# Optimization experiments

Hardware: AMD Instinct MI355X
Metric: run time of the kernel (lower is better)

## Reference

```python
import jax, jax.numpy as jnp
import numpy as np

N, C, H, W, D = 2, 64, 256, 256, 2   # batch, dim, height, width, depth
NW, HEADS, TOPK, KVW = 8, 8, 4, 4    # n_win, num_heads, topk, kv_per_win


def _conv(x, w, b, pad, groups=1):
    # x: NCHW, w: OIHW
    y = jax.lax.conv_general_dilated(
        x, w, (1, 1), [(pad, pad), (pad, pad)],
        dimension_numbers=('NCHW', 'OIHW', 'NCHW'), feature_group_count=groups)
    return y if b is None else y + b[None, :, None, None]


def _ln(x, g, b):
    m = x.mean(-1, keepdims=True)
    v = ((x - m) ** 2).mean(-1, keepdims=True)
    return (x - m) * jax.lax.rsqrt(v + 1e-6) * g + b


def setup_inputs() -> dict:
    key = jax.random.key(0)
    ks = iter(jax.random.split(key, 32))
    def rn(shape, s=0.05):
        return jax.random.normal(next(ks), shape, jnp.float32) * s
    inp = {'x': jax.random.normal(next(ks), (N, C, H, W), jnp.float32)}
    inp.update(
        pos_w=rn((D, C, 1, 3, 3)), pos_b=jnp.zeros((D, C), jnp.float32),
        ln1_g=jnp.ones((D, C), jnp.float32), ln1_b=jnp.zeros((D, C), jnp.float32),
        qkv_w=rn((D, C, 3 * C)), qkv_b=jnp.zeros((D, 3 * C), jnp.float32),
        lepe_w=rn((D, C, 1, 5, 5)), lepe_b=jnp.zeros((D, C), jnp.float32),
        wo_w=rn((D, C, C)), wo_b=jnp.zeros((D, C), jnp.float32),
        ln2_g=jnp.ones((D, C), jnp.float32), ln2_b=jnp.zeros((D, C), jnp.float32),
        fc1_w=rn((D, C, 4 * C)), fc1_b=jnp.zeros((D, 4 * C), jnp.float32),
        pw_w=rn((D, 2 * C, 2 * C, 1, 1)),
        dw_w=rn((D, 2 * C, 1, 3, 3)), dw_b=jnp.zeros((D, 2 * C), jnp.float32),
        fc2_w=rn((D, 2 * C, C)), fc2_b=jnp.zeros((D, C), jnp.float32))
    return inp


def _attn(y, qkv_w, qkv_b, lepe_w, lepe_b, wo_w, wo_b):
    # Bi-level routing attention. y: NHWC
    n, h, w, c = y.shape
    hw, ww = h // NW, w // NW          # window size (32x32)
    p2 = NW * NW                        # number of windows (64)
    hd = c // HEADS
    scale = c ** -0.5                   # qk_dim ** -0.5
    qkv = y @ qkv_w + qkv_b             # (n,h,w,3c)
    q, kimg, vimg = jnp.split(qkv, 3, -1)

    def win(t):  # (n,h,w,c) -> (n,p2,hw,ww,c)
        return t.reshape(n, NW, hw, NW, ww, c).transpose(0, 1, 3, 2, 4, 5).reshape(n, p2, hw, ww, c)

    qw, kw, vw = win(q), win(kimg), win(vimg)
    # region-level routing: window-mean q/k, top-k windows per query window
    q_win = qw.mean((2, 3))
    k_win = kw.mean((2, 3))
    logits = jnp.einsum('npc,nqc->npq', q_win * scale, k_win)
    _, r_idx = jax.lax.top_k(logits, TOPK)           # (n,p2,topk) hard routing (mul_weight='none')
    # kv downsample: adaptive avg pool each 32x32 window to 4x4
    kv = jnp.concatenate([kw, vw], -1)               # (n,p2,hw,ww,2c)
    kvp = kv.reshape(n, p2, KVW, hw // KVW, KVW, ww // KVW, 2 * c).mean((3, 5))
    kvp = kvp.reshape(n, p2, KVW * KVW, 2 * c)       # (n,p2,16,2c)
    # gather top-k windows' kv tokens
    kv_sel = jax.vmap(lambda t, i: t[i])(kvp, r_idx)  # (n,p2,topk,16,2c)
    k_sel, v_sel = jnp.split(kv_sel, 2, -1)
    kt = TOPK * KVW * KVW                             # 64 kv tokens per window
    k_sel = k_sel.reshape(n, p2, kt, HEADS, hd)
    v_sel = v_sel.reshape(n, p2, kt, HEADS, hd)
    qp = qw.reshape(n, p2, hw * ww, HEADS, hd)
    att = jax.nn.softmax(jnp.einsum('npqhc,npkhc->nphqk', qp * scale, k_sel), -1)
    out = jnp.einsum('nphqk,npkhc->npqhc', att, v_sel).reshape(n, p2, hw, ww, c)
    out = out.reshape(n, NW, NW, hw, ww, c).transpose(0, 1, 3, 2, 4, 5).reshape(n, h, w, c)
    # LePE: depthwise 5x5 conv on v over the full image
    lepe = _conv(vimg.transpose(0, 3, 1, 2), lepe_w, lepe_b, 2, groups=c).transpose(0, 2, 3, 1)
    return (out + lepe) @ wo_w + wo_b


def _glu(y, fc1_w, fc1_b, pw_w, dw_w, dw_b, fc2_w, fc2_b):
    # BConvolutionalGLU. y: NHWC
    t = y @ fc1_w + fc1_b                 # (n,h,w,4c)
    xh, vh = jnp.split(t, 2, -1)          # each 2c
    xh = xh.transpose(0, 3, 1, 2)         # NCHW
    xh = _conv(xh, pw_w, None, 0)                           # BSConvU pointwise (no bias)
    xh = _conv(xh, dw_w, dw_b, 1, groups=dw_w.shape[0])     # BSConvU depthwise 3x3
    xh = jax.nn.gelu(xh, approximate=False) * vh.transpose(0, 3, 1, 2)
    return xh.transpose(0, 2, 3, 1) @ fc2_w + fc2_b


def reference(x, pos_w, pos_b, ln1_g, ln1_b, qkv_w, qkv_b, lepe_w, lepe_b,
              wo_w, wo_b, ln2_g, ln2_b, fc1_w, fc1_b, pw_w, dw_w, dw_b,
              fc2_w, fc2_b):
    for i in range(D):
        x = x + _conv(x, pos_w[i], pos_b[i], 1, groups=x.shape[1])
        y = x.transpose(0, 2, 3, 1)  # NHWC
        y = y + _attn(_ln(y, ln1_g[i], ln1_b[i]), qkv_w[i], qkv_b[i],
                      lepe_w[i], lepe_b[i], wo_w[i], wo_b[i])
        y = y + _glu(_ln(y, ln2_g[i], ln2_b[i]), fc1_w[i], fc1_b[i],
                     pw_w[i], dw_w[i], dw_b[i], fc2_w[i], fc2_b[i])
        x = y.transpose(0, 3, 1, 2)  # NCHW
    return x
```

## Files before the change

kernel.cpp:

```cpp
#include <hip/hip_runtime.h>
#include <hip/hip_bf16.h>

typedef __hip_bfloat16 bf16;
typedef __attribute__((ext_vector_type(8))) short short8v;
typedef __attribute__((ext_vector_type(4))) float f32x4;

static constexpr int Nn = 2, Hh = 256, Wd = 256;
static constexpr int Pp = Nn * Hh * Wd;

__device__ inline void sto(float* p, size_t i, float v) { p[i] = v; }
__device__ inline void sto(bf16* p, size_t i, float v) { p[i] = __float2bfloat16(v); }
__device__ inline void ld4(const float* p, float f[4]) {
  const float4 v = *(const float4*)p;
  f[0] = v.x; f[1] = v.y; f[2] = v.z; f[3] = v.w;
}
__device__ inline void ld4(const bf16* p, float f[4]) {
  uint2 u = *(const uint2*)p;
  f[0] = __uint_as_float(u.x << 16); f[1] = __uint_as_float(u.x & 0xffff0000u);
  f[2] = __uint_as_float(u.y << 16); f[3] = __uint_as_float(u.y & 0xffff0000u);
}
__device__ inline void st4(float* p, const float f[4]) {
  *(float4*)p = make_float4(f[0], f[1], f[2], f[3]);
}
__device__ inline void st4(bf16* p, const float f[4]) {
  union { bf16 h[4]; uint2 u; } x;
  x.h[0] = __float2bfloat16(f[0]); x.h[1] = __float2bfloat16(f[1]);
  x.h[2] = __float2bfloat16(f[2]); x.h[3] = __float2bfloat16(f[3]);
  *(uint2*)p = x.u;
}
__device__ inline uint2 pk4(float a, float b, float c, float d) {
  union { bf16 h[4]; uint2 u; } x;
  x.h[0] = __float2bfloat16(a); x.h[1] = __float2bfloat16(b);
  x.h[2] = __float2bfloat16(c); x.h[3] = __float2bfloat16(d);
  return x.u;
}

__global__ void __launch_bounds__(256) k_in_tr(const float* __restrict__ xin,
                                               float* __restrict__ X) {
  __shared__ float t[64][65];
  int blk = blockIdx.x;
  int wt = blk & 3, h = (blk >> 2) & 255, n = blk >> 10;
  int w0 = wt * 64;
  int tx = threadIdx.x & 63, ty = threadIdx.x >> 6;
  const float* src = xin + ((size_t)n * 64 * 256 + h) * 256 + w0;
#pragma unroll
  for (int cc = 0; cc < 16; cc++) {
    int c = cc * 4 + ty;
    t[c][tx] = src[(size_t)c * 65536 + tx];
  }
  __syncthreads();
  float* dst = X + (size_t)(n * 65536 + h * 256 + w0) * 64;
#pragma unroll
  for (int jj = 0; jj < 16; jj++) {
    int j = jj * 4 + ty;
    dst[(size_t)j * 64 + tx] = t[tx][j];
  }
}

__global__ void __launch_bounds__(256) k_out(const float* __restrict__ X,
                                             float* __restrict__ out) {
  __shared__ float t[64][65];
  int blk = blockIdx.x;
  int wt = blk & 3, h = (blk >> 2) & 255, n = blk >> 10;
  int w0 = wt * 64;
  int tx = threadIdx.x & 63, ty = threadIdx.x >> 6;
  const float* src = X + (size_t)(n * 65536 + h * 256 + w0) * 64;
#pragma unroll
  for (int jj = 0; jj < 16; jj++) {
    int j = jj * 4 + ty;
    t[tx][j] = src[(size_t)j * 64 + tx];
  }
  __syncthreads();
  float* dst = out + ((size_t)n * 64 * 256 + h) * 256 + w0;
#pragma unroll
  for (int cc = 0; cc < 16; cc++) {
    int c = cc * 4 + ty;
    dst[(size_t)c * 65536 + tx] = t[c][tx];
  }
}

__global__ void __launch_bounds__(256) k_pcln4(const float* __restrict__ X,
                                               float* __restrict__ A, float* __restrict__ T,
                                               bf16* __restrict__ Tb,
                                               const float* __restrict__ pw,
                                               const float* __restrict__ pb,
                                               const float* __restrict__ g,
                                               const float* __restrict__ b) {
  __shared__ float w9[9][68];
  __shared__ float bb[64];
  int tid = threadIdx.x;
  for (int j = tid; j < 576; j += 256) {
    int tap = j >> 6, c = j & 63;
    w9[tap][c] = pw[c * 9 + tap];
  }
  if (tid < 64) bb[tid] = pb[tid];
  __syncthreads();
  int gid = blockIdx.x * 256 + tid;
  int cg = gid & 15, pg = gid >> 4;
  int c0 = cg << 2;
  int w0 = (pg & 63) << 2, h = (pg >> 6) & 255, n = pg >> 14;
  int pbase = (n << 16) | (h << 8) | w0;
  float acc[4][4];
  {
    const float4 b4 = *(const float4*)&bb[c0];
#pragma unroll
    for (int px = 0; px < 4; px++) {
      acc[px][0] = b4.x; acc[px][1] = b4.y; acc[px][2] = b4.z; acc[px][3] = b4.w;
    }
  }
  float xc[4][4];
#pragma unroll
  for (int ky = 0; ky < 3; ky++) {
    int hh = h + ky - 1;
    if ((unsigned)hh >= 256u) continue;
    const float* xrow = X + (size_t)((n << 16) | (hh << 8)) * 64 + c0;
    float v[6][4];
#pragma unroll
    for (int dx = 0; dx < 6; dx++) {
      int ww = w0 + dx - 1;
      if ((unsigned)ww < 256u) ld4(xrow + (size_t)ww * 64, v[dx]);
      else { v[dx][0] = 0.f; v[dx][1] = 0.f; v[dx][2] = 0.f; v[dx][3] = 0.f; }
    }
    if (ky == 1) {
#pragma unroll
      for (int px = 0; px < 4; px++)
#pragma unroll
        for (int j = 0; j < 4; j++) xc[px][j] = v[px + 1][j];
    }
#pragma unroll
    for (int kx = 0; kx < 3; kx++) {
      const float4 wv = *(const float4*)&w9[ky * 3 + kx][c0];
#pragma unroll
      for (int px = 0; px < 4; px++) {
        acc[px][0] += wv.x * v[px + kx][0]; acc[px][1] += wv.y * v[px + kx][1];
        acc[px][2] += wv.z * v[px + kx][2]; acc[px][3] += wv.w * v[px + kx][3];
      }
    }
  }
  const float4 g4 = *(const float4*)&g[c0];
  const float4 b4 = *(const float4*)&b[c0];
#pragma unroll
  for (int px = 0; px < 4; px++) {
    float a[4];
#pragma unroll
    for (int j = 0; j < 4; j++) a[j] = xc[px][j] + acc[px][j];
    st4(A + (size_t)(pbase + px) * 64 + c0, a);
    float s = a[0] + a[1] + a[2] + a[3];
#pragma unroll
    for (int off = 8; off; off >>= 1) s += __shfl_xor(s, off);
    float mean = s * (1.f / 64.f);
    float d[4], q = 0.f;
#pragma unroll
    for (int j = 0; j < 4; j++) { d[j] = a[j] - mean; q += d[j] * d[j]; }
#pragma unroll
    for (int off = 8; off; off >>= 1) q += __shfl_xor(q, off);
    float inv = rsqrtf(q * (1.f / 64.f) + 1e-6f);
    float y[4] = {d[0] * inv * g4.x + b4.x, d[1] * inv * g4.y + b4.y,
                  d[2] * inv * g4.z + b4.z, d[3] * inv * g4.w + b4.w};
    st4(T + (size_t)(pbase + px) * 64 + c0, y);
    st4(Tb + (size_t)(pbase + px) * 64 + c0, y);
  }
}

__global__ void k_prep(const float* __restrict__ qkvw, const float* __restrict__ qkvb,
                       const float* __restrict__ wow, const float* __restrict__ f2w,
                       const float* __restrict__ f1w, const float* __restrict__ f1b,
                       const float* __restrict__ pww,
                       bf16* __restrict__ WTq, bf16* __restrict__ WTo,
                       bf16* __restrict__ WT2, bf16* __restrict__ WTf1,
                       float* __restrict__ qbs, float* __restrict__ bc) {
  int t = blockIdx.x * 256 + threadIdx.x;
  if (t < 8192) {
    int r = t >> 6, k = t & 63;
    int src = r < 64 ? r : r + 64;
    float v = qkvw[k * 192 + src];
    if (r < 64) v *= 0.125f;
    WTq[t] = __float2bfloat16(v);
  } else if (t < 12288) {
    int t2 = t - 8192;
    int r = t2 >> 6, k = t2 & 63;
    WTo[t2] = __float2bfloat16(wow[k * 64 + r]);
  } else if (t < 20480) {
    int t2 = t - 12288;
    int r = t2 >> 7, k = t2 & 127;
    WT2[t2] = __float2bfloat16(f2w[k * 64 + r]);
  } else if (t < 28672) {
    int t2 = t - 20480;
    int r = t2 >> 6, k = t2 & 63;
    WTf1[t2] = __float2bfloat16(f1w[k * 256 + 128 + r]);
  } else if (t < 36864) {
    int t2 = t - 28672;
    int o = t2 & 127, k = t2 >> 7;
    float acc = 0.f;
    for (int j = 0; j < 128; j++) acc += f1w[k * 256 + j] * pww[o * 128 + j];
    WTf1[(128 + o) * 64 + k] = __float2bfloat16(acc);
  } else if (t < 36992) {
    int o = t - 36864;
    float bv = 0.f;
    for (int j = 0; j < 128; j++) bv += f1b[j] * pww[o * 128 + j];
    bc[o] = bv;
  }
  if (t < 64) qbs[t] = qkvb[t] * 0.125f;
}

template <int K, int N1, int N2, typename TO1, typename TO2, bool RES>
__global__ void __launch_bounds__(256) k_mf(const bf16* __restrict__ In,
                                            const bf16* __restrict__ WT,
                                            const float* __restrict__ b1,
                                            const float* __restrict__ b2,
                                            const float* __restrict__ Res,
                                            TO1* __restrict__ O1, TO2* __restrict__ O2) {
  constexpr int NC = N1 + N2;
  constexpr int KS = K / 32;
  constexpr int NTW = NC / 64;
  constexpr int KB = K * 2;
  constexpr int CH = NC * K / 8;
  __shared__ char lw[NC * K * 2];
  int tid = threadIdx.x;
  for (int ch = tid; ch < CH; ch += 256) {
    int r = ch / (K / 8), cg = ch % (K / 8);
    int byte = (r * KB + cg * 16) ^ ((r & 7) << 4);
    *(uint4*)(lw + byte) = *(const uint4*)((const short*)WT + ch * 8);
  }
  __syncthreads();
  int wid = tid >> 6, lane = tid & 63;
  int lr = lane & 15, lg = lane >> 4;
  int mb = blockIdx.x * 128;
#pragma unroll 2
  for (int ms = 0; ms < 8; ms++) {
    int m0 = mb + ms * 16;
    short8v a[KS];
#pragma unroll
    for (int ks = 0; ks < KS; ks++)
      a[ks] = *(const short8v*)((const short*)In + (size_t)(m0 + lr) * K + ks * 32 + lg * 8);
#pragma unroll
    for (int t = 0; t < NTW; t++) {
      int nt = wid * NTW + t;
      int col = nt * 16 + lr;
      float bv = (N2 == 0 || col < N1) ? b1[col] : b2[col - N1];
      f32x4 acc = {bv, bv, bv, bv};
#pragma unroll
      for (int ks = 0; ks < KS; ks++) {
        int byte = (col * KB + ks * 64 + lg * 16) ^ ((col & 7) << 4);
        short8v bfrag = *(const short8v*)(lw + byte);
        acc = __builtin_amdgcn_mfma_f32_16x16x32_bf16(a[ks], bfrag, acc, 0, 0, 0);
      }
      int r0 = m0 + lg * 4;
#pragma unroll
      for (int j = 0; j < 4; j++) {
        float v = acc[j];
        size_t row = r0 + j;
        if (RES) v += Res[row * N1 + col];
        if (N2 == 0 || col < N1) sto(O1, row * N1 + col, v);
        else sto(O2, row * N2 + (col - N1), v);
      }
    }
  }
}

__global__ void __launch_bounds__(256) k_mf_wo_ln(const bf16* __restrict__ In,
                                                  const bf16* __restrict__ WT,
                                                  const float* __restrict__ bias,
                                                  const float* __restrict__ Res,
                                                  float* __restrict__ Xo,
                                                  bf16* __restrict__ A2b,
                                                  const float* __restrict__ g,
                                                  const float* __restrict__ b) {
  __shared__ char lw[64 * 64 * 2];
  __shared__ float xs[16][68];
  int tid = threadIdx.x;
  for (int ch = tid; ch < 512; ch += 256) {
    int r = ch >> 3, cg = ch & 7;
    int byte = (r * 128 + cg * 16) ^ ((r & 7) << 4);
    *(uint4*)(lw + byte) = *(const uint4*)((const short*)WT + ch * 8);
  }
  __syncthreads();
  int wid = tid >> 6, lane = tid & 63;
  int lr = lane & 15, lg = lane >> 4;
  int col = wid * 16 + lr;
  int mb = blockIdx.x * 128;
  int row2 = tid >> 4, cq = (tid & 15) << 2;
  const float4 g4 = *(const float4*)&g[cq];
  const float4 b4 = *(const float4*)&b[cq];
  float bv = bias[col];
  for (int ms = 0; ms < 8; ms++) {
    int m0 = mb + ms * 16;
    short8v a0 = *(const short8v*)((const short*)In + (size_t)(m0 + lr) * 64 + lg * 8);
    short8v a1 = *(const short8v*)((const short*)In + (size_t)(m0 + lr) * 64 + 32 + lg * 8);
    f32x4 acc = {bv, bv, bv, bv};
    {
      int byte = (col * 128 + lg * 16) ^ ((col & 7) << 4);
      acc = __builtin_amdgcn_mfma_f32_16x16x32_bf16(a0, *(const short8v*)(lw + byte), acc, 0, 0, 0);
      byte = (col * 128 + 64 + lg * 16) ^ ((col & 7) << 4);
      acc = __builtin_amdgcn_mfma_f32_16x16x32_bf16(a1, *(const short8v*)(lw + byte), acc, 0, 0, 0);
    }
    int r0 = m0 + lg * 4;
#pragma unroll
    for (int j = 0; j < 4; j++) {
      float v = acc[j] + Res[(size_t)(r0 + j) * 64 + col];
      Xo[(size_t)(r0 + j) * 64 + col] = v;
      xs[lg * 4 + j][col] = v;
    }
    __syncthreads();
    {
      float a4[4] = {xs[row2][cq], xs[row2][cq + 1], xs[row2][cq + 2], xs[row2][cq + 3]};
      float s = a4[0] + a4[1] + a4[2] + a4[3];
#pragma unroll
      for (int off = 8; off; off >>= 1) s += __shfl_xor(s, off);
      float mean = s * (1.f / 64.f);
      float d[4], q = 0.f;
#pragma unroll
      for (int j = 0; j < 4; j++) { d[j] = a4[j] - mean; q += d[j] * d[j]; }
#pragma unroll
      for (int off = 8; off; off >>= 1) q += __shfl_xor(q, off);
      float inv = rsqrtf(q * (1.f / 64.f) + 1e-6f);
      float y[4] = {d[0] * inv * g4.x + b4.x, d[1] * inv * g4.y + b4.y,
                    d[2] * inv * g4.z + b4.z, d[3] * inv * g4.w + b4.w};
      st4(A2b + (size_t)(m0 + row2) * 64 + cq, y);
    }
    __syncthreads();
  }
}

__global__ void k_pool8(const float* __restrict__ T, float* __restrict__ Y8) {
  int b = blockIdx.x;
  int c = threadIdx.x;
  int bx = b & 31, by = (b >> 5) & 31, n = b >> 10;
  float acc = 0.f;
  for (int r = 0; r < 8; r++)
    for (int s = 0; s < 8; s++) {
      int p = (n << 16) | ((by * 8 + r) << 8) | (bx * 8 + s);
      acc += T[(size_t)p * 64 + c];
    }
  Y8[(size_t)b * 64 + c] = acc * (1.f / 64.f);
}

__global__ void __launch_bounds__(256) k_qkwin2(const float* __restrict__ Y8,
                                                const float* __restrict__ qw,
                                                const float* __restrict__ qb,
                                                float* __restrict__ QW,
                                                float* __restrict__ KW) {
  __shared__ float ym[4][68];
  int blk = blockIdx.x;
  int sel = blk >> 5;
  int r0 = (blk & 31) * 4;
  int tid = threadIdx.x;
  {
    int rl = tid >> 6, c = tid & 63;
    int row = r0 + rl;
    int n = row >> 6, win = row & 63;
    int wi = win >> 3, wj = win & 7;
    float acc = 0.f;
    for (int ti = 0; ti < 4; ti++)
      for (int tj = 0; tj < 4; tj++) {
        int y8 = (n * 32 + wi * 4 + ti) * 32 + wj * 4 + tj;
        acc += Y8[(size_t)y8 * 64 + c];
      }
    ym[rl][c] = acc * (1.f / 16.f);
  }
  __syncthreads();
  int rl = tid >> 6, c = tid & 63;
  int row = r0 + rl;
  int colg = sel * 64 + c;
  float acc = qb[colg];
  for (int k = 0; k < 64; k++) acc += ym[rl][k] * qw[k * 192 + colg];
  (sel ? KW : QW)[(size_t)row * 64 + c] = acc;
}

__global__ void k_kvp(const float* __restrict__ Y8, const float* __restrict__ qw,
                      const float* __restrict__ qb, float* __restrict__ KVP) {
  int t = blockIdx.x * blockDim.x + threadIdx.x;
  if (t >= 262144) return;
  int c2 = t & 127, tok = (t >> 7) & 15, win = (t >> 11) & 63, n = t >> 17;
  int wi = win >> 3, wj = win & 7, ti = tok >> 2, tj = tok & 3;
  int y8 = (n * 32 + wi * 4 + ti) * 32 + wj * 4 + tj;
  const float* y = Y8 + (size_t)y8 * 64;
  int col = 64 + c2;
  float acc = qb[col];
  for (int k = 0; k < 64; k++) acc += y[k] * qw[k * 192 + col];
  KVP[t] = acc;
}

__global__ void __launch_bounds__(64) k_route(const float* __restrict__ QW,
                                              const float* __restrict__ KW,
                                              int* __restrict__ RIDX) {
  __shared__ float kk[64][65];
  __shared__ float qq[64];
  int b = blockIdx.x;
  int lane = threadIdx.x;
  int n = b >> 6;
  qq[lane] = QW[(size_t)b * 64 + lane];
  for (int r = 0; r < 64; r++) kk[r][lane] = KW[(size_t)(n * 64 + r) * 64 + lane];
  __syncthreads();
  float t = 0.f;
  for (int c = 0; c < 64; c++) t += qq[c] * kk[lane][c];
  t *= 0.125f;
  int o0 = 0, o1 = 0, o2 = 0, o3 = 0;
#pragma unroll
  for (int j = 0; j < 4; j++) {
    float v = t; int idx = lane;
#pragma unroll
    for (int off = 32; off; off >>= 1) {
      float ov = __shfl_xor(v, off);
      int oi = __shfl_xor(idx, off);
      if (ov > v || (ov == v && oi < idx)) { v = ov; idx = oi; }
    }
    if (j == 0) o0 = idx; else if (j == 1) o1 = idx;
    else if (j == 2) o2 = idx; else o3 = idx;
    if (lane == idx) t = -1e30f;
  }
  if (lane == 0) {
    int* o = RIDX + (size_t)b * 4;
    o[0] = o0; o[1] = o1; o[2] = o2; o[3] = o3;
  }
}

__global__ void __launch_bounds__(256) k_attn_mf(const bf16* __restrict__ Qb,
                                                 const float* __restrict__ KVP,
                                                 const int* __restrict__ RIDX,
                                                 bf16* __restrict__ Sbf) {
  __shared__ bf16 ks[64][72];
  __shared__ bf16 vt[64][72];
  __shared__ bf16 pa[4][16][72];
  __shared__ float ldn[4][16];
  __shared__ int idx[4];
  int blk = blockIdx.x;
  int part = blk & 3, bw = blk >> 2;
  int n = bw >> 6, win = bw & 63;
  int tid = threadIdx.x;
  if (tid < 4) idx[tid] = RIDX[bw * 4 + tid];
  __syncthreads();
  {
    int tok = tid & 63;
    const float* src = KVP + ((size_t)(n * 64 + idx[tok >> 4]) * 16 + (tok & 15)) * 128;
    for (int cq = tid >> 6; cq < 16; cq += 4) {
      int c0 = cq * 4;
      const float4 k4 = *(const float4*)&src[c0];
      *(uint2*)&ks[tok][c0] = pk4(k4.x, k4.y, k4.z, k4.w);
      const float4 v4 = *(const float4*)&src[64 + c0];
      vt[c0 + 0][tok] = __float2bfloat16(v4.x);
      vt[c0 + 1][tok] = __float2bfloat16(v4.y);
      vt[c0 + 2][tok] = __float2bfloat16(v4.z);
      vt[c0 + 3][tok] = __float2bfloat16(v4.w);
    }
  }
  __syncthreads();
  int w = tid >> 6, lane = tid & 63;
  int lr = lane & 15, lg = lane >> 4;
  int wi = win >> 3, wj = win & 7;
  for (int it = 0; it < 4; it++) {
    int qbase = part * 256 + w * 64 + it * 16;
    int q_b = qbase + lr;
    int pix_b = (n << 16) | ((wi * 32 + (q_b >> 5)) << 8) | (wj * 32 + (q_b & 31));
    short8v qf0 = *(const short8v*)((const short*)Qb + (size_t)pix_b * 64 + lg * 8);
    short8v qf1 = *(const short8v*)((const short*)Qb + (size_t)pix_b * 64 + 32 + lg * 8);
    f32x4 p[4] = {{0,0,0,0},{0,0,0,0},{0,0,0,0},{0,0,0,0}};
#pragma unroll
    for (int mt = 0; mt < 4; mt++) {
      short8v a0 = *(const short8v*)&ks[mt * 16 + lr][lg * 8];
      p[mt] = __builtin_amdgcn_mfma_f32_16x16x32_bf16(a0, qf0, p[mt], 0, 0, 0);
    }
#pragma unroll
    for (int mt = 0; mt < 4; mt++) {
      short8v a1 = *(const short8v*)&ks[mt * 16 + lr][32 + lg * 8];
      p[mt] = __builtin_amdgcn_mfma_f32_16x16x32_bf16(a1, qf1, p[mt], 0, 0, 0);
    }
    float mx = -1e30f;
#pragma unroll
    for (int mt = 0; mt < 4; mt++)
#pragma unroll
      for (int j = 0; j < 4; j++) mx = fmaxf(mx, p[mt][j]);
    mx = fmaxf(mx, __shfl_xor(mx, 16));
    mx = fmaxf(mx, __shfl_xor(mx, 32));
    float e[4][4];
    float sum = 0.f;
#pragma unroll
    for (int mt = 0; mt < 4; mt++)
#pragma unroll
      for (int j = 0; j < 4; j++) { e[mt][j] = __expf(p[mt][j] - mx); sum += e[mt][j]; }
    sum += __shfl_xor(sum, 16);
    sum += __shfl_xor(sum, 32);
    if (lg == 0) ldn[w][lr] = sum;
#pragma unroll
    for (int mt = 0; mt < 4; mt++)
      *(uint2*)&pa[w][lr][mt * 16 + lg * 4] = pk4(e[mt][0], e[mt][1], e[mt][2], e[mt][3]);
    short8v pf0 = *(const short8v*)&pa[w][lr][lg * 8];
    short8v pf1 = *(const short8v*)&pa[w][lr][32 + lg * 8];
    f32x4 o4[4] = {{0,0,0,0},{0,0,0,0},{0,0,0,0},{0,0,0,0}};
#pragma unroll
    for (int nt = 0; nt < 4; nt++) {
      short8v v0 = *(const short8v*)&vt[nt * 16 + lr][lg * 8];
      o4[nt] = __builtin_amdgcn_mfma_f32_16x16x32_bf16(pf0, v0, o4[nt], 0, 0, 0);
    }
#pragma unroll
    for (int nt = 0; nt < 4; nt++) {
      short8v v1 = *(const short8v*)&vt[nt * 16 + lr][32 + lg * 8];
      o4[nt] = __builtin_amdgcn_mfma_f32_16x16x32_bf16(pf1, v1, o4[nt], 0, 0, 0);
    }
    float linv[4];
#pragma unroll
    for (int j = 0; j < 4; j++) linv[j] = 1.f / ldn[w][lg * 4 + j];
#pragma unroll
    for (int j = 0; j < 4; j++) {
      int q_o = qbase + lg * 4 + j;
      size_t pix_o = (n << 16) | ((wi * 32 + (q_o >> 5)) << 8) | (wj * 32 + (q_o & 31));
      bf16* op = Sbf + pix_o * 64 + lr;
#pragma unroll
      for (int nt = 0; nt < 4; nt++) op[nt * 16] = __float2bfloat16(o4[nt][j] * linv[j]);
    }
  }
}

__global__ void __launch_bounds__(256) k_lepe4(const bf16* __restrict__ V,
                                               const bf16* __restrict__ Sbf,
                                               bf16* __restrict__ Sb,
                                               const float* __restrict__ wt,
                                               const float* __restrict__ bs) {
  __shared__ float w5[25][68];
  __shared__ float bb[64];
  int tid = threadIdx.x;
  for (int j = tid; j < 1600; j += 256) {
    int tap = j >> 6, c = j & 63;
    w5[tap][c] = wt[c * 25 + tap];
  }
  if (tid < 64) bb[tid] = bs[tid];
  __syncthreads();
  int gid = blockIdx.x * 256 + tid;
  int cg = gid & 15, pg = gid >> 4;
  int c0 = cg << 2;
  int w0 = (pg & 63) << 2, h = (pg >> 6) & 255, n = pg >> 14;
  int pbase = (n << 16) | (h << 8) | w0;
  float acc[4][4];
  {
    const float4 b4 = *(const float4*)&bb[c0];
#pragma unroll
    for (int px = 0; px < 4; px++) {
      acc[px][0] = b4.x; acc[px][1] = b4.y; acc[px][2] = b4.z; acc[px][3] = b4.w;
    }
  }
#pragma unroll
  for (int ky = 0; ky < 5; ky++) {
    int hh = h + ky - 2;
    if ((unsigned)hh >= 256u) continue;
    const bf16* vrow = V + (size_t)((n << 16) | (hh << 8)) * 64 + c0;
    float v[8][4];
#pragma unroll
    for (int dx = 0; dx < 8; dx++) {
      int ww = w0 + dx - 2;
      if ((unsigned)ww < 256u) ld4(vrow + (size_t)ww * 64, v[dx]);
      else { v[dx][0] = 0.f; v[dx][1] = 0.f; v[dx][2] = 0.f; v[dx][3] = 0.f; }
    }
#pragma unroll
    for (int kx = 0; kx < 5; kx++) {
      const float4 wv = *(const float4*)&w5[ky * 5 + kx][c0];
#pragma unroll
      for (int px = 0; px < 4; px++) {
        acc[px][0] += wv.x * v[px + kx][0]; acc[px][1] += wv.y * v[px + kx][1];
        acc[px][2] += wv.z * v[px + kx][2]; acc[px][3] += wv.w * v[px + kx][3];
      }
    }
  }
#pragma unroll
  for (int px = 0; px < 4; px++) {
    float s4[4];
    ld4(Sbf + (size_t)(pbase + px) * 64 + c0, s4);
    float o[4] = {s4[0] + acc[px][0], s4[1] + acc[px][1],
                  s4[2] + acc[px][2], s4[3] + acc[px][3]};
    st4(Sb + (size_t)(pbase + px) * 64 + c0, o);
  }
}

__global__ void __launch_bounds__(256) k_gludw4(const bf16* __restrict__ PWO,
                                                const bf16* __restrict__ VH,
                                                const float* __restrict__ wt,
                                                const float* __restrict__ bs,
                                                bf16* __restrict__ G) {
  __shared__ float wd[9][132];
  __shared__ float bb[128];
  int tid = threadIdx.x;
  for (int j = tid; j < 1152; j += 256) {
    int tap = j >> 7, c = j & 127;
    wd[tap][c] = wt[c * 9 + tap];
  }
  if (tid < 128) bb[tid] = bs[tid];
  __syncthreads();
  int gid = blockIdx.x * 256 + tid;
  int cg = gid & 31, pg = gid >> 5;
  int c0 = cg << 2;
  int w0 = (pg & 63) << 2, h = (pg >> 6) & 255, n = pg >> 14;
  int pbase = (n << 16) | (h << 8) | w0;
  float acc[4][4];
  {
    const float4 b4 = *(const float4*)&bb[c0];
#pragma unroll
    for (int px = 0; px < 4; px++) {
      acc[px][0] = b4.x; acc[px][1] = b4.y; acc[px][2] = b4.z; acc[px][3] = b4.w;
    }
  }
#pragma unroll
  for (int ky = 0; ky < 3; ky++) {
    int hh = h + ky - 1;
    if ((unsigned)hh >= 256u) continue;
    const bf16* prow = PWO + (size_t)((n << 16) | (hh << 8)) * 128 + c0;
    float v[6][4];
#pragma unroll
    for (int dx = 0; dx < 6; dx++) {
      int ww = w0 + dx - 1;
      if ((unsigned)ww < 256u) ld4(prow + (size_t)ww * 128, v[dx]);
      else { v[dx][0] = 0.f; v[dx][1] = 0.f; v[dx][2] = 0.f; v[dx][3] = 0.f; }
    }
#pragma unroll
    for (int kx = 0; kx < 3; kx++) {
      const float4 wv = *(const float4*)&wd[ky * 3 + kx][c0];
#pragma unroll
      for (int px = 0; px < 4; px++) {
        acc[px][0] += wv.x * v[px + kx][0]; acc[px][1] += wv.y * v[px + kx][1];
        acc[px][2] += wv.z * v[px + kx][2]; acc[px][3] += wv.w * v[px + kx][3];
      }
    }
  }
#pragma unroll
  for (int px = 0; px < 4; px++) {
    float vh[4];
    ld4(VH + (size_t)(pbase + px) * 128 + c0, vh);
    float o[4];
#pragma unroll
    for (int j = 0; j < 4; j++) {
      float x = acc[px][j];
      float ge = 0.5f * x * (1.f + erff(x * 0.70710678118f));
      o[j] = ge * vh[j];
    }
    st4(G + (size_t)(pbase + px) * 128 + c0, o);
  }
}

extern "C" void kernel_launch(void* const* d_in, const int* in_sizes, int n_in,
                              void* d_out, int out_size, void* d_ws, size_t ws_size,
                              hipStream_t stream) {
  (void)in_sizes; (void)n_in; (void)out_size; (void)ws_size;
  const float* xin = (const float*)d_in[0];
  auto Wp = [&](int i) { return (const float*)d_in[i]; };
  char* ws = (char*)d_ws;
  const size_t MB = 1u << 20;
  float* X  = (float*)(ws + 0 * MB);
  float* A  = (float*)(ws + 32 * MB);
  float* T  = (float*)(ws + 64 * MB);
  char*  sm = ws + 128 * MB;
  size_t off = 0;
  auto alloc = [&](size_t bytes) {
    void* p = sm + off;
    off += (bytes + 255) & ~(size_t)255;
    return p;
  };
  float* Y8   = (float*)alloc(2 * 32 * 32 * 64 * 4);
  float* QW   = (float*)alloc(2 * 64 * 64 * 4);
  float* KW   = (float*)alloc(2 * 64 * 64 * 4);
  float* KVP  = (float*)alloc(2 * 64 * 16 * 128 * 4);
  int*  RIDX  = (int*)alloc(2 * 64 * 4 * 4);
  float* bc   = (float*)alloc(128 * 4);
  bf16* WTq   = (bf16*)alloc(128 * 64 * 2);
  bf16* WTo   = (bf16*)alloc(64 * 64 * 2);
  bf16* WT2   = (bf16*)alloc(64 * 128 * 2);
  bf16* WTf1  = (bf16*)alloc(256 * 64 * 2);
  float* qbs  = (float*)alloc(64 * 4);
  bf16* Qb   = (bf16*)X;
  bf16* Vb   = (bf16*)(ws + 96 * MB);
  bf16* Tb   = (bf16*)(ws + 112 * MB);
  bf16* Sbf  = (bf16*)T;
  bf16* Sb   = Tb;
  bf16* A2b  = (bf16*)(ws + 96 * MB);
  bf16* VH   = (bf16*)A;
  bf16* PWO  = (bf16*)T;
  bf16* G    = (bf16*)(ws + 96 * MB);

  k_in_tr<<<dim3(2048), dim3(256), 0, stream>>>(xin, X);
  for (int i = 0; i < 2; i++) {
    const float *posw = Wp(1) + i * 64 * 9, *posb = Wp(2) + i * 64;
    const float *l1g = Wp(3) + i * 64, *l1b = Wp(4) + i * 64;
    const float *qkvw = Wp(5) + i * 64 * 192, *qkvb = Wp(6) + i * 192;
    const float *lpw = Wp(7) + i * 64 * 25, *lpb = Wp(8) + i * 64;
    const float *wow = Wp(9) + i * 64 * 64, *wob = Wp(10) + i * 64;
    const float *l2g = Wp(11) + i * 64, *l2b = Wp(12) + i * 64;
    const float *f1w = Wp(13) + i * 64 * 256, *f1b = Wp(14) + i * 256;
    const float *pww = Wp(15) + i * 128 * 128;
    const float *dww = Wp(16) + i * 128 * 9, *dwb = Wp(17) + i * 128;
    const float *f2w = Wp(18) + i * 128 * 64, *f2b = Wp(19) + i * 64;

    k_prep<<<dim3(145), dim3(256), 0, stream>>>(qkvw, qkvb, wow, f2w, f1w, f1b, pww,
                                                WTq, WTo, WT2, WTf1, qbs, bc);
    k_pcln4<<<dim3(2048), dim3(256), 0, stream>>>(X, A, T, Tb, posw, posb, l1g, l1b);
    k_mf<64, 64, 64, bf16, bf16, false><<<dim3(Pp / 128), dim3(256), 0, stream>>>(
        Tb, WTq, qbs, qkvb + 128, nullptr, Qb, Vb);
    k_pool8<<<dim3(2048), dim3(64), 0, stream>>>(T, Y8);
    k_qkwin2<<<dim3(64), dim3(256), 0, stream>>>(Y8, qkvw, qkvb, QW, KW);
    k_kvp<<<dim3(1024), dim3(256), 0, stream>>>(Y8, qkvw, qkvb, KVP);
    k_route<<<dim3(128), dim3(64), 0, stream>>>(QW, KW, RIDX);
    k_attn_mf<<<dim3(512), dim3(256), 0, stream>>>(Qb, KVP, RIDX, Sbf);
    k_lepe4<<<dim3(2048), dim3(256), 0, stream>>>(Vb, Sbf, Sb, lpw, lpb);
    k_mf_wo_ln<<<dim3(Pp / 128), dim3(256), 0, stream>>>(
        Sb, WTo, wob, A, X, A2b, l2g, l2b);
    k_mf<64, 128, 128, bf16, bf16, false><<<dim3(Pp / 128), dim3(256), 0, stream>>>(
        A2b, WTf1, f1b + 128, bc, nullptr, VH, PWO);
    k_gludw4<<<dim3(4096), dim3(256), 0, stream>>>(PWO, VH, dww, dwb, G);
    k_mf<128, 64, 0, float, float, true><<<dim3(Pp / 128), dim3(256), 0, stream>>>(
        G, WT2, f2b, nullptr, X, X, nullptr);
  }
  k_out<<<dim3(2048), dim3(256), 0, stream>>>(X, (float*)d_out);
}
```

Baseline: 448.7 us.

## Fuse QKV GEMM into pos-conv+LN, fc1 into wo+LN, fc2 into GLU depthwise

Three separate MFMA GEMM kernels are folded into their producer stages. The qkv projection now runs on LN1 output staged in shared memory, fc1 runs on LN2 output staged per 16-row tile, and fc2 runs on the gated depthwise output held in shared memory. This drops the bf16 intermediates Tb, A2b and G along with their global round trips and three launches. In exchange the fused kernels use much more shared memory, which may reduce occupancy, and they add extra barriers.

```diff
diff --git a/kernel.cpp b/kernel.cpp
--- a/kernel.cpp
+++ b/kernel.cpp
@@ -8,8 +8,6 @@
 static constexpr int Nn = 2, Hh = 256, Wd = 256;
 static constexpr int Pp = Nn * Hh * Wd;
 
-__device__ inline void sto(float* p, size_t i, float v) { p[i] = v; }
-__device__ inline void sto(bf16* p, size_t i, float v) { p[i] = __float2bfloat16(v); }
 __device__ inline void ld4(const float* p, float f[4]) {
   const float4 v = *(const float4*)p;
   f[0] = v.x; f[1] = v.y; f[2] = v.z; f[3] = v.w;
@@ -79,27 +77,41 @@
   }
 }
 
-__global__ void __launch_bounds__(256) k_pcln4(const float* __restrict__ X,
-                                               float* __restrict__ A, float* __restrict__ T,
-                                               bf16* __restrict__ Tb,
-                                               const float* __restrict__ pw,
-                                               const float* __restrict__ pb,
-                                               const float* __restrict__ g,
-                                               const float* __restrict__ b) {
+__global__ void __launch_bounds__(256) k_pcln_qkv(const float* __restrict__ X,
+                                                  float* __restrict__ A,
+                                                  float* __restrict__ T,
+                                                  const float* __restrict__ pw,
+                                                  const float* __restrict__ pb,
+                                                  const float* __restrict__ g,
+                                                  const float* __restrict__ b,
+                                                  const bf16* __restrict__ WTq,
+                                                  const float* __restrict__ qbs,
+                                                  const float* __restrict__ vbias,
+                                                  bf16* __restrict__ Qb,
+                                                  bf16* __restrict__ Vb) {
   __shared__ float w9[9][68];
   __shared__ float bb[64];
+  __shared__ bf16 yt[64][72];
+  __shared__ char lw[128 * 64 * 2];
   int tid = threadIdx.x;
   for (int j = tid; j < 576; j += 256) {
     int tap = j >> 6, c = j & 63;
     w9[tap][c] = pw[c * 9 + tap];
   }
   if (tid < 64) bb[tid] = pb[tid];
-  __syncthreads();
-  int gid = blockIdx.x * 256 + tid;
+  for (int ch = tid; ch < 1024; ch += 256) {
+    int r = ch >> 3, cg = ch & 7;
+    int byte = (r * 128 + cg * 16) ^ ((r & 7) << 4);
+    *(uint4*)(lw + byte) = *(const uint4*)((const short*)WTq + ch * 8);
+  }
+  __syncthreads();
+  int blk = blockIdx.x;
+  int gid = blk * 256 + tid;
   int cg = gid & 15, pg = gid >> 4;
   int c0 = cg << 2;
   int w0 = (pg & 63) << 2, h = (pg >> 6) & 255, n = pg >> 14;
   int pbase = (n << 16) | (h << 8) | w0;
+  int pl0 = (tid >> 4) << 2;
   float acc[4][4];
   {
     const float4 b4 = *(const float4*)&bb[c0];
@@ -158,7 +170,29 @@
     float y[4] = {d[0] * inv * g4.x + b4.x, d[1] * inv * g4.y + b4.y,
                   d[2] * inv * g4.z + b4.z, d[3] * inv * g4.w + b4.w};
     st4(T + (size_t)(pbase + px) * 64 + c0, y);
-    st4(Tb + (size_t)(pbase + px) * 64 + c0, y);
+    st4(&yt[pl0 + px][c0], y);
+  }
+  __syncthreads();
+  int wid = tid >> 6, lane = tid & 63;
+  int lr = lane & 15, lg = lane >> 4;
+  size_t mbase = (size_t)blk * 64;
+  short8v a0 = *(const short8v*)&yt[wid * 16 + lr][lg * 8];
+  short8v a1 = *(const short8v*)&yt[wid * 16 + lr][32 + lg * 8];
+#pragma unroll
+  for (int nt = 0; nt < 8; nt++) {
+    int col = nt * 16 + lr;
+    float bv = col < 64 ? qbs[col] : vbias[col - 64];
+    f32x4 acc4 = {bv, bv, bv, bv};
+    int byte = (col * 128 + lg * 16) ^ ((col & 7) << 4);
+    acc4 = __builtin_amdgcn_mfma_f32_16x16x32_bf16(a0, *(const short8v*)(lw + byte), acc4, 0, 0, 0);
+    byte = (col * 128 + 64 + lg * 16) ^ ((col & 7) << 4);
+    acc4 = __builtin_amdgcn_mfma_f32_16x16x32_bf16(a1, *(const short8v*)(lw + byte), acc4, 0, 0, 0);
+#pragma unroll
+    for (int j = 0; j < 4; j++) {
+      size_t pix = mbase + wid * 16 + lg * 4 + j;
+      if (col < 64) Qb[pix * 64 + col] = __float2bfloat16(acc4[j]);
+      else          Vb[pix * 64 + (col - 64)] = __float2bfloat16(acc4[j]);
+    }
   }
 }
 
@@ -203,103 +237,58 @@
   if (t < 64) qbs[t] = qkvb[t] * 0.125f;
 }
 
-template <int K, int N1, int N2, typename TO1, typename TO2, bool RES>
-__global__ void __launch_bounds__(256) k_mf(const bf16* __restrict__ In,
-                                            const bf16* __restrict__ WT,
-                                            const float* __restrict__ b1,
-                                            const float* __restrict__ b2,
-                                            const float* __restrict__ Res,
-                                            TO1* __restrict__ O1, TO2* __restrict__ O2) {
-  constexpr int NC = N1 + N2;
-  constexpr int KS = K / 32;
-  constexpr int NTW = NC / 64;
-  constexpr int KB = K * 2;
-  constexpr int CH = NC * K / 8;
-  __shared__ char lw[NC * K * 2];
-  int tid = threadIdx.x;
-  for (int ch = tid; ch < CH; ch += 256) {
-    int r = ch / (K / 8), cg = ch % (K / 8);
-    int byte = (r * KB + cg * 16) ^ ((r & 7) << 4);
-    *(uint4*)(lw + byte) = *(const uint4*)((const short*)WT + ch * 8);
-  }
-  __syncthreads();
-  int wid = tid >> 6, lane = tid & 63;
-  int lr = lane & 15, lg = lane >> 4;
-  int mb = blockIdx.x * 128;
-#pragma unroll 2
-  for (int ms = 0; ms < 8; ms++) {
-    int m0 = mb + ms * 16;
-    short8v a[KS];
-#pragma unroll
-    for (int ks = 0; ks < KS; ks++)
-      a[ks] = *(const short8v*)((const short*)In + (size_t)(m0 + lr) * K + ks * 32 + lg * 8);
-#pragma unroll
-    for (int t = 0; t < NTW; t++) {
-      int nt = wid * NTW + t;
-      int col = nt * 16 + lr;
-      float bv = (N2 == 0 || col < N1) ? b1[col] : b2[col - N1];
-      f32x4 acc = {bv, bv, bv, bv};
-#pragma unroll
-      for (int ks = 0; ks < KS; ks++) {
-        int byte = (col * KB + ks * 64 + lg * 16) ^ ((col & 7) << 4);
-        short8v bfrag = *(const short8v*)(lw + byte);
-        acc = __builtin_amdgcn_mfma_f32_16x16x32_bf16(a[ks], bfrag, acc, 0, 0, 0);
-      }
-      int r0 = m0 + lg * 4;
-#pragma unroll
-      for (int j = 0; j < 4; j++) {
-        float v = acc[j];
-        size_t row = r0 + j;
-        if (RES) v += Res[row * N1 + col];
-        if (N2 == 0 || col < N1) sto(O1, row * N1 + col, v);
-        else sto(O2, row * N2 + (col - N1), v);
-      }
-    }
-  }
-}
-
-__global__ void __launch_bounds__(256) k_mf_wo_ln(const bf16* __restrict__ In,
-                                                  const bf16* __restrict__ WT,
-                                                  const float* __restrict__ bias,
-                                                  const float* __restrict__ Res,
-                                                  float* __restrict__ Xo,
-                                                  bf16* __restrict__ A2b,
-                                                  const float* __restrict__ g,
-                                                  const float* __restrict__ b) {
-  __shared__ char lw[64 * 64 * 2];
+__global__ void __launch_bounds__(256) k_wo_ln_fc1(const bf16* __restrict__ In,
+                                                   const bf16* __restrict__ WTo,
+                                                   const float* __restrict__ wob,
+                                                   const float* __restrict__ Res,
+                                                   float* __restrict__ Xo,
+                                                   const float* __restrict__ g,
+                                                   const float* __restrict__ b,
+                                                   const bf16* __restrict__ WTf1,
+                                                   const float* __restrict__ b1,
+                                                   const float* __restrict__ b2,
+                                                   bf16* __restrict__ VH,
+                                                   bf16* __restrict__ PWO) {
+  __shared__ char lwo[64 * 64 * 2];
+  __shared__ char lf1[256 * 64 * 2];
   __shared__ float xs[16][68];
+  __shared__ bf16 a2t[16][72];
   int tid = threadIdx.x;
   for (int ch = tid; ch < 512; ch += 256) {
     int r = ch >> 3, cg = ch & 7;
     int byte = (r * 128 + cg * 16) ^ ((r & 7) << 4);
-    *(uint4*)(lw + byte) = *(const uint4*)((const short*)WT + ch * 8);
+    *(uint4*)(lwo + byte) = *(const uint4*)((const short*)WTo + ch * 8);
+  }
+  for (int ch = tid; ch < 2048; ch += 256) {
+    int r = ch >> 3, cg = ch & 7;
+    int byte = (r * 128 + cg * 16) ^ ((r & 7) << 4);
+    *(uint4*)(lf1 + byte) = *(const uint4*)((const short*)WTf1 + ch * 8);
   }
   __syncthreads();
   int wid = tid >> 6, lane = tid & 63;
   int lr = lane & 15, lg = lane >> 4;
-  int col = wid * 16 + lr;
+  int col_o = wid * 16 + lr;
   int mb = blockIdx.x * 128;
   int row2 = tid >> 4, cq = (tid & 15) << 2;
   const float4 g4 = *(const float4*)&g[cq];
   const float4 b4 = *(const float4*)&b[cq];
-  float bv = bias[col];
+  float bvo = wob[col_o];
   for (int ms = 0; ms < 8; ms++) {
     int m0 = mb + ms * 16;
-    short8v a0 = *(const short8v*)((const short*)In + (size_t)(m0 + lr) * 64 + lg * 8);
-    short8v a1 = *(const short8v*)((const short*)In + (size_t)(m0 + lr) * 64 + 32 + lg * 8);
-    f32x4 acc = {bv, bv, bv, bv};
     {
-      int byte = (col * 128 + lg * 16) ^ ((col & 7) << 4);
-      acc = __builtin_amdgcn_mfma_f32_16x16x32_bf16(a0, *(const short8v*)(lw + byte), acc, 0, 0, 0);
-      byte = (col * 128 + 64 + lg * 16) ^ ((col & 7) << 4);
-      acc = __builtin_amdgcn_mfma_f32_16x16x32_bf16(a1, *(const short8v*)(lw + byte), acc, 0, 0, 0);
-    }
-    int r0 = m0 + lg * 4;
-#pragma unroll
-    for (int j = 0; j < 4; j++) {
-      float v = acc[j] + Res[(size_t)(r0 + j) * 64 + col];
-      Xo[(size_t)(r0 + j) * 64 + col] = v;
-      xs[lg * 4 + j][col] = v;
+      short8v a0 = *(const short8v*)((const short*)In + (size_t)(m0 + lr) * 64 + lg * 8);
+      short8v a1 = *(const short8v*)((const short*)In + (size_t)(m0 + lr) * 64 + 32 + lg * 8);
+      f32x4 acc = {bvo, bvo, bvo, bvo};
+      int byte = (col_o * 128 + lg * 16) ^ ((col_o & 7) << 4);
+      acc = __builtin_amdgcn_mfma_f32_16x16x32_bf16(a0, *(const short8v*)(lwo + byte), acc, 0, 0, 0);
+      byte = (col_o * 128 + 64 + lg * 16) ^ ((col_o & 7) << 4);
+      acc = __builtin_amdgcn_mfma_f32_16x16x32_bf16(a1, *(const short8v*)(lwo + byte), acc, 0, 0, 0);
+#pragma unroll
+      for (int j = 0; j < 4; j++) {
+        float v = acc[j] + Res[(size_t)(m0 + lg * 4 + j) * 64 + col_o];
+        Xo[(size_t)(m0 + lg * 4 + j) * 64 + col_o] = v;
+        xs[lg * 4 + j][col_o] = v;
+      }
     }
     __syncthreads();
     {
@@ -316,9 +305,135 @@
       float inv = rsqrtf(q * (1.f / 64.f) + 1e-6f);
       float y[4] = {d[0] * inv * g4.x + b4.x, d[1] * inv * g4.y + b4.y,
                     d[2] * inv * g4.z + b4.z, d[3] * inv * g4.w + b4.w};
-      st4(A2b + (size_t)(m0 + row2) * 64 + cq, y);
+      st4(&a2t[row2][cq], y);
     }
     __syncthreads();
+    {
+      short8v f0 = *(const short8v*)&a2t[lr][lg * 8];
+      short8v f1 = *(const short8v*)&a2t[lr][32 + lg * 8];
+#pragma unroll
+      for (int t = 0; t < 4; t++) {
+        int nt = wid * 4 + t;
+        int col = nt * 16 + lr;
+        float bv = col < 128 ? b1[col] : b2[col - 128];
+        f32x4 acc = {bv, bv, bv, bv};
+        int byte = (col * 128 + lg * 16) ^ ((col & 7) << 4);
+        acc = __builtin_amdgcn_mfma_f32_16x16x32_bf16(f0, *(const short8v*)(lf1 + byte), acc, 0, 0, 0);
+        byte = (col * 128 + 64 + lg * 16) ^ ((col & 7) << 4);
+        acc = __builtin_amdgcn_mfma_f32_16x16x32_bf16(f1, *(const short8v*)(lf1 + byte), acc, 0, 0, 0);
+#pragma unroll
+        for (int j = 0; j < 4; j++) {
+          size_t pix = m0 + lg * 4 + j;
+          if (col < 128) VH[pix * 128 + col] = __float2bfloat16(acc[j]);
+          else           PWO[pix * 128 + (col - 128)] = __float2bfloat16(acc[j]);
+        }
+      }
+    }
+    __syncthreads();
+  }
+}
+
+__global__ void __launch_bounds__(256) k_glu_fc2(const bf16* __restrict__ PWO,
+                                                 const bf16* __restrict__ VH,
+                                                 const float* __restrict__ wt,
+                                                 const float* __restrict__ bs,
+                                                 const bf16* __restrict__ WT2,
+                                                 const float* __restrict__ f2b,
+                                                 float* __restrict__ X) {
+  __shared__ float wd[9][132];
+  __shared__ float bb[128];
+  __shared__ bf16 gt[128][136];
+  __shared__ char lw2[64 * 128 * 2];
+  int tid = threadIdx.x;
+  for (int j = tid; j < 1152; j += 256) {
+    int tap = j >> 7, c = j & 127;
+    wd[tap][c] = wt[c * 9 + tap];
+  }
+  if (tid < 128) bb[tid] = bs[tid];
+  for (int ch = tid; ch < 1024; ch += 256) {
+    int r = ch >> 4, cg = ch & 15;
+    int byte = (r * 256 + cg * 16) ^ ((r & 7) << 4);
+    *(uint4*)(lw2 + byte) = *(const uint4*)((const short*)WT2 + ch * 8);
+  }
+  __syncthreads();
+  int blk = blockIdx.x;
+  int w0 = (blk & 1) * 128, h = (blk >> 1) & 255, n = blk >> 9;
+  int pbase = (n << 16) | (h << 8) | w0;
+  int cg = tid & 31, c0 = cg << 2;
+  int pg = tid >> 5;
+  const float4 bb4 = *(const float4*)&bb[c0];
+#pragma unroll
+  for (int pass = 0; pass < 4; pass++) {
+    int wb = w0 + pass * 32 + pg * 4;
+    float acc[4][4];
+#pragma unroll
+    for (int px = 0; px < 4; px++) {
+      acc[px][0] = bb4.x; acc[px][1] = bb4.y; acc[px][2] = bb4.z; acc[px][3] = bb4.w;
+    }
+#pragma unroll
+    for (int ky = 0; ky < 3; ky++) {
+      int hh = h + ky - 1;
+      if ((unsigned)hh >= 256u) continue;
+      const bf16* prow = PWO + (size_t)((n << 16) | (hh << 8)) * 128 + c0;
+      float v[6][4];
+#pragma unroll
+      for (int dx = 0; dx < 6; dx++) {
+        int ww = wb + dx - 1;
+        if ((unsigned)ww < 256u) ld4(prow + (size_t)ww * 128, v[dx]);
+        else { v[dx][0] = 0.f; v[dx][1] = 0.f; v[dx][2] = 0.f; v[dx][3] = 0.f; }
+      }
+#pragma unroll
+      for (int kx = 0; kx < 3; kx++) {
+        const float4 wv = *(const float4*)&wd[ky * 3 + kx][c0];
+#pragma unroll
+        for (int px = 0; px < 4; px++) {
+          acc[px][0] += wv.x * v[px + kx][0]; acc[px][1] += wv.y * v[px + kx][1];
+          acc[px][2] += wv.z * v[px + kx][2]; acc[px][3] += wv.w * v[px + kx][3];
+        }
+      }
+    }
+#pragma unroll
+    for (int px = 0; px < 4; px++) {
+      int pl = pass * 32 + pg * 4 + px;
+      float vh[4];
+      ld4(VH + (size_t)(pbase + pl) * 128 + c0, vh);
+      float o[4];
+#pragma unroll
+      for (int j = 0; j < 4; j++) {
+        float x = acc[px][j];
+        float ge = 0.5f * x * (1.f + erff(x * 0.70710678118f));
+        o[j] = ge * vh[j];
+      }
+      st4(&gt[pl][c0], o);
+    }
+  }
+  __syncthreads();
+  int wid = tid >> 6, lane = tid & 63;
+  int lr = lane & 15, lg = lane >> 4;
+#pragma unroll
+  for (int mi = 0; mi < 2; mi++) {
+    int mt = wid + mi * 4;
+    int m0 = mt * 16;
+    short8v a[4];
+#pragma unroll
+    for (int ks = 0; ks < 4; ks++)
+      a[ks] = *(const short8v*)&gt[m0 + lr][ks * 32 + lg * 8];
+#pragma unroll
+    for (int nt = 0; nt < 4; nt++) {
+      int col = nt * 16 + lr;
+      float bv = f2b[col];
+      f32x4 acc = {bv, bv, bv, bv};
+#pragma unroll
+      for (int ks = 0; ks < 4; ks++) {
+        int byte = (col * 256 + ks * 64 + lg * 16) ^ ((col & 7) << 4);
+        acc = __builtin_amdgcn_mfma_f32_16x16x32_bf16(a[ks], *(const short8v*)(lw2 + byte), acc, 0, 0, 0);
+      }
+#pragma unroll
+      for (int j = 0; j < 4; j++) {
+        size_t pix = pbase + m0 + lg * 4 + j;
+        X[pix * 64 + col] += acc[j];
+      }
+    }
   }
 }
 
@@ -567,70 +682,6 @@
     float o[4] = {s4[0] + acc[px][0], s4[1] + acc[px][1],
                   s4[2] + acc[px][2], s4[3] + acc[px][3]};
     st4(Sb + (size_t)(pbase + px) * 64 + c0, o);
-  }
-}
-
-__global__ void __launch_bounds__(256) k_gludw4(const bf16* __restrict__ PWO,
-                                                const bf16* __restrict__ VH,
-                                                const float* __restrict__ wt,
-                                                const float* __restrict__ bs,
-                                                bf16* __restrict__ G) {
-  __shared__ float wd[9][132];
-  __shared__ float bb[128];
-  int tid = threadIdx.x;
-  for (int j = tid; j < 1152; j += 256) {
-    int tap = j >> 7, c = j & 127;
-    wd[tap][c] = wt[c * 9 + tap];
-  }
-  if (tid < 128) bb[tid] = bs[tid];
-  __syncthreads();
-  int gid = blockIdx.x * 256 + tid;
-  int cg = gid & 31, pg = gid >> 5;
-  int c0 = cg << 2;
-  int w0 = (pg & 63) << 2, h = (pg >> 6) & 255, n = pg >> 14;
-  int pbase = (n << 16) | (h << 8) | w0;
-  float acc[4][4];
-  {
-    const float4 b4 = *(const float4*)&bb[c0];
-#pragma unroll
-    for (int px = 0; px < 4; px++) {
-      acc[px][0] = b4.x; acc[px][1] = b4.y; acc[px][2] = b4.z; acc[px][3] = b4.w;
-    }
-  }
-#pragma unroll
-  for (int ky = 0; ky < 3; ky++) {
-    int hh = h + ky - 1;
-    if ((unsigned)hh >= 256u) continue;
-    const bf16* prow = PWO + (size_t)((n << 16) | (hh << 8)) * 128 + c0;
-    float v[6][4];
-#pragma unroll
-    for (int dx = 0; dx < 6; dx++) {
-      int ww = w0 + dx - 1;
-      if ((unsigned)ww < 256u) ld4(prow + (size_t)ww * 128, v[dx]);
-      else { v[dx][0] = 0.f; v[dx][1] = 0.f; v[dx][2] = 0.f; v[dx][3] = 0.f; }
-    }
-#pragma unroll
-    for (int kx = 0; kx < 3; kx++) {
-      const float4 wv = *(const float4*)&wd[ky * 3 + kx][c0];
-#pragma unroll
-      for (int px = 0; px < 4; px++) {
-        acc[px][0] += wv.x * v[px + kx][0]; acc[px][1] += wv.y * v[px + kx][1];
-        acc[px][2] += wv.z * v[px + kx][2]; acc[px][3] += wv.w * v[px + kx][3];
-      }
-    }
-  }
-#pragma unroll
-  for (int px = 0; px < 4; px++) {
-    float vh[4];
-    ld4(VH + (size_t)(pbase + px) * 128 + c0, vh);
-    float o[4];
-#pragma unroll
-    for (int j = 0; j < 4; j++) {
-      float x = acc[px][j];
-      float ge = 0.5f * x * (1.f + erff(x * 0.70710678118f));
-      o[j] = ge * vh[j];
-    }
-    st4(G + (size_t)(pbase + px) * 128 + c0, o);
   }
 }
 
@@ -663,15 +714,12 @@
   bf16* WT2   = (bf16*)alloc(64 * 128 * 2);
   bf16* WTf1  = (bf16*)alloc(256 * 64 * 2);
   float* qbs  = (float*)alloc(64 * 4);
-  bf16* Qb   = (bf16*)X;
   bf16* Vb   = (bf16*)(ws + 96 * MB);
-  bf16* Tb   = (bf16*)(ws + 112 * MB);
+  bf16* Qb   = (bf16*)(ws + 112 * MB);
   bf16* Sbf  = (bf16*)T;
-  bf16* Sb   = Tb;
-  bf16* A2b  = (bf16*)(ws + 96 * MB);
+  bf16* Sb   = (bf16*)(ws + 112 * MB);
   bf16* VH   = (bf16*)A;
   bf16* PWO  = (bf16*)T;
-  bf16* G    = (bf16*)(ws + 96 * MB);
 
   k_in_tr<<<dim3(2048), dim3(256), 0, stream>>>(xin, X);
   for (int i = 0; i < 2; i++) {
@@ -688,22 +736,17 @@
 
     k_prep<<<dim3(145), dim3(256), 0, stream>>>(qkvw, qkvb, wow, f2w, f1w, f1b, pww,
                                                 WTq, WTo, WT2, WTf1, qbs, bc);
-    k_pcln4<<<dim3(2048), dim3(256), 0, stream>>>(X, A, T, Tb, posw, posb, l1g, l1b);
-    k_mf<64, 64, 64, bf16, bf16, false><<<dim3(Pp / 128), dim3(256), 0, stream>>>(
-        Tb, WTq, qbs, qkvb + 128, nullptr, Qb, Vb);
+    k_pcln_qkv<<<dim3(2048), dim3(256), 0, stream>>>(
+        X, A, T, posw, posb, l1g, l1b, WTq, qbs, qkvb + 128, Qb, Vb);
     k_pool8<<<dim3(2048), dim3(64), 0, stream>>>(T, Y8);
     k_qkwin2<<<dim3(64), dim3(256), 0, stream>>>(Y8, qkvw, qkvb, QW, KW);
     k_kvp<<<dim3(1024), dim3(256), 0, stream>>>(Y8, qkvw, qkvb, KVP);
     k_route<<<dim3(128), dim3(64), 0, stream>>>(QW, KW, RIDX);
     k_attn_mf<<<dim3(512), dim3(256), 0, stream>>>(Qb, KVP, RIDX, Sbf);
     k_lepe4<<<dim3(2048), dim3(256), 0, stream>>>(Vb, Sbf, Sb, lpw, lpb);
-    k_mf_wo_ln<<<dim3(Pp / 128), dim3(256), 0, stream>>>(
-        Sb, WTo, wob, A, X, A2b, l2g, l2b);
-    k_mf<64, 128, 128, bf16, bf16, false><<<dim3(Pp / 128), dim3(256), 0, stream>>>(
-        A2b, WTf1, f1b + 128, bc, nullptr, VH, PWO);
-    k_gludw4<<<dim3(4096), dim3(256), 0, stream>>>(PWO, VH, dww, dwb, G);
-    k_mf<128, 64, 0, float, float, true><<<dim3(Pp / 128), dim3(256), 0, stream>>>(
-        G, WT2, f2b, nullptr, X, X, nullptr);
+    k_wo_ln_fc1<<<dim3(Pp / 128), dim3(256), 0, stream>>>(
+        Sb, WTo, wob, A, X, l2g, l2b, WTf1, f1b + 128, bc, VH, PWO);
+    k_glu_fc2<<<dim3(1024), dim3(256), 0, stream>>>(PWO, VH, dww, dwb, WT2, f2b, X);
   }
   k_out<<<dim3(2048), dim3(256), 0, stream>>>(X, (float*)d_out);
 }
```

Result: no change. 441.4 us (-1.6%).
